# Kernel tuning notes

Measured on AMD Instinct MI355X. Metric: run time of the kernel, lower is better.

## Reference

```python
import jax, jax.numpy as jnp
import numpy as np

B, T, H, W, C = 2, 8, 64, 64, 128
NH, KT, KH, KW = 4, 3, 7, 7
HD = C // NH
SCALE = HD ** -0.5


def _starts(L, ks):
    i = jnp.arange(L)
    return jnp.clip(i - ks // 2, 0, L - ks)  # NATTEN border-clamped window start


def _na3d(q, k, v, rpb):
    # q,k,v: [B,T,H,W,NH,HD]; rpb: [NH,2KT-1,2KH-1,2KW-1]
    st, sh, sw = _starts(T, KT), _starts(H, KH), _starts(W, KW)
    ot, oh, ow = jnp.meshgrid(jnp.arange(KT), jnp.arange(KH), jnp.arange(KW), indexing='ij')
    ot, oh, ow = ot.ravel(), oh.ravel(), ow.ravel()          # [K] kernel offsets, K=KT*KH*KW
    t_abs = st[None, :] + ot[:, None]                        # [K,T] absolute neighbor coords
    h_abs = sh[None, :] + oh[:, None]                        # [K,H]
    w_abs = sw[None, :] + ow[:, None]                        # [K,W]
    qs = q * SCALE
    it, ih, iw = jnp.arange(T), jnp.arange(H), jnp.arange(W)

    def score_step(_, idx):
        ta, ha, wa = idx
        kg = k[:, ta][:, :, ha][:, :, :, wa]                 # [B,T,H,W,NH,HD] shifted keys
        s = jnp.einsum('bthwnd,bthwnd->bthwn', qs, kg)
        rt = ta - it + (KT - 1)
        rh = ha - ih + (KH - 1)
        rw = wa - iw + (KW - 1)
        bias = rpb[:, rt][:, :, rh][:, :, :, rw]             # [NH,T,H,W]
        return None, s + jnp.transpose(bias, (1, 2, 3, 0))[None]

    _, scores = jax.lax.scan(score_step, None, (t_abs, h_abs, w_abs))  # [K,B,T,H,W,NH]
    attn = jax.nn.softmax(scores, axis=0)

    def av_step(acc, xs):
        a, ta, ha, wa = xs
        vg = v[:, ta][:, :, ha][:, :, :, wa]                 # [B,T,H,W,NH,HD]
        return acc + a[..., None] * vg, None

    out, _ = jax.lax.scan(av_step, jnp.zeros_like(q), (attn, t_abs, h_abs, w_abs))
    return out


def setup_inputs() -> dict:
    key = jax.random.key(0)
    ks = jax.random.split(key, 6)
    x = jax.random.normal(ks[0], (B, T, H, W, C), jnp.float32)
    y = jax.random.normal(ks[1], (B, T, H, W, C), jnp.float32)
    qv_w = jax.random.normal(ks[2], (C, 2 * C), jnp.float32) * 0.02
    qv_b = jnp.zeros((2 * C,), jnp.float32)
    k_w = jax.random.normal(ks[3], (C, C), jnp.float32) * 0.02
    k_b = jnp.zeros((C,), jnp.float32)
    proj_w = jax.random.normal(ks[4], (C, C), jnp.float32) * 0.02
    proj_b = jnp.zeros((C,), jnp.float32)
    rpb = jax.random.normal(ks[5], (NH, 2 * KT - 1, 2 * KH - 1, 2 * KW - 1), jnp.float32) * 0.02
    return {'x': x, 'y': y, 'qv_w': qv_w, 'qv_b': qv_b, 'k_w': k_w, 'k_b': k_b,
            'proj_w': proj_w, 'proj_b': proj_b, 'rpb': rpb}


def reference(x, y, qv_w, qv_b, k_w, k_b, proj_w, proj_b, rpb):
    qv = (x @ qv_w + qv_b).reshape(B, T, H, W, 2, NH, HD)
    q, v = qv[..., 0, :, :], qv[..., 1, :, :]
    k = (y @ k_w + k_b).reshape(B, T, H, W, NH, HD)
    o = _na3d(q, k, v, rpb).reshape(B, T, H, W, C)
    return o @ proj_w + proj_b
```

## Files before the change

kernel.cpp:

```cpp
#include <hip/hip_runtime.h>
#include <hip/hip_bf16.h>
#include <hip/hip_fp16.h>
#include <cmath>

#define Bv   2
#define Tv   8
#define Hv   64
#define Wv   64
#define MPOS (Bv*Tv*Hv*Wv)
#define SCALEv 0.17677669529663687f

#define U_H   14
#define U_W   14
#define UPOS  588

#define KOFF   0
#define VTOFF  37888
#define POFF2  77312
#define RPBOFF 158720
#define SMEM_BYTES 162112

#define KPAD 136

typedef __attribute__((ext_vector_type(8))) short bf16x8;
typedef __attribute__((ext_vector_type(4))) float f32x4;

__device__ __forceinline__ unsigned short f2bf16(float x) {
  return __builtin_bit_cast(unsigned short, __float2bfloat16(x));
}
__device__ __forceinline__ float bf2f(unsigned short h) {
  return __uint_as_float((unsigned)h << 16);
}
__device__ __forceinline__ float h2f(unsigned short h) {
  return __half2float(__builtin_bit_cast(__half, h));
}
__device__ __forceinline__ unsigned short f2h(float x) {
  return __builtin_bit_cast(unsigned short, __float2half(x));
}
__device__ __forceinline__ unsigned pk2(float a, float b) {
  return (unsigned)f2bf16(a) | ((unsigned)f2bf16(b) << 16);
}
__device__ __forceinline__ void gload_lds16(const void* gsrc, void* ldst) {
  __builtin_amdgcn_global_load_lds(
      (const __attribute__((address_space(1))) unsigned int*)gsrc,
      (__attribute__((address_space(3))) unsigned int*)ldst, 16, 0, 0);
}

__global__ __launch_bounds__(256) void preconvert(
    const float* __restrict__ qv_w, const float* __restrict__ k_w,
    const float* __restrict__ proj_w,
    ushort* __restrict__ wqvT, ushort* __restrict__ wkT,
    ushort* __restrict__ wpT_hi, ushort* __restrict__ wpT_lo) {
  const int id = blockIdx.x * 256 + threadIdx.x;
  if (id < 32768) {
    const int n = id >> 7, kk = id & 127;
    wqvT[n * KPAD + kk] = f2bf16(qv_w[kk * 256 + n]);
  } else if (id < 49152) {
    const int j = id - 32768;
    const int n = j >> 7, kk = j & 127;
    wkT[n * KPAD + kk] = f2bf16(k_w[kk * 128 + n]);
  } else {
    const int j = id - 49152;
    const int n = j >> 7, kk = j & 127;
    const float v = proj_w[kk * 128 + n];
    const unsigned short hi = f2bf16(v);
    wpT_hi[n * KPAD + kk] = hi;
    wpT_lo[n * KPAD + kk] = f2bf16(v - bf2f(hi));
  }
}

__global__ __launch_bounds__(512) void gemm_qvk(
    const float* __restrict__ x, const float* __restrict__ y,
    const ushort* __restrict__ wqvT, const ushort* __restrict__ wkT,
    const float* __restrict__ qv_b, const float* __restrict__ k_b,
    ushort* __restrict__ qbuf, ushort* __restrict__ vbuf,
    ushort* __restrict__ kbuf) {
  __shared__ ushort Ws[128 * KPAD];
  const int tid  = threadIdx.x;
  const int bx   = blockIdx.x;
  const int seg  = bx >> 9;
  const int row0 = (bx & 511) * 128;

  const float*  A    = (seg == 2) ? y : x;
  const ushort* W    = (seg == 0) ? wqvT : (seg == 1) ? wqvT + 128 * KPAD : wkT;
  const float*  bias = (seg == 0) ? qv_b : (seg == 1) ? qv_b + 128 : k_b;
  ushort*       outp = (seg == 0) ? qbuf : (seg == 1) ? vbuf : kbuf;
  const float   scale = (seg == 0) ? SCALEv : 1.0f;

  {
    const uint4* wg = (const uint4*)W;
    for (int i = tid; i < 2176; i += 512)
      gload_lds16(wg + i, (uint4*)Ws + i);
  }

  const int wv = tid >> 6, lane = tid & 63, quad = lane >> 4, l16 = lane & 15;
  const int arow = row0 + wv * 16 + l16;

  bf16x8 af[4];
#pragma unroll
  for (int kk = 0; kk < 4; ++kk) {
    const float4* ap = (const float4*)(A + (size_t)arow * 128 + kk * 32 + quad * 8);
    const float4 a = ap[0], b2 = ap[1];
    af[kk] = __builtin_bit_cast(bf16x8,
        make_uint4(pk2(a.x, a.y), pk2(a.z, a.w), pk2(b2.x, b2.y), pk2(b2.z, b2.w)));
  }
  __syncthreads();

  f32x4 C[8];
#pragma unroll
  for (int nt = 0; nt < 8; ++nt) C[nt] = (f32x4){0.f, 0.f, 0.f, 0.f};

#pragma unroll
  for (int kk = 0; kk < 4; ++kk) {
#pragma unroll
    for (int nt = 0; nt < 8; ++nt) {
      const bf16x8 b2 = *(const bf16x8*)(Ws + (nt * 16 + l16) * KPAD + kk * 32 + quad * 8);
      C[nt] = __builtin_amdgcn_mfma_f32_16x16x32_bf16(af[kk], b2, C[nt], 0, 0, 0);
    }
  }

#pragma unroll
  for (int nt = 0; nt < 8; ++nt) {
    const int col = nt * 16 + l16;
    const float bv = bias[col];
#pragma unroll
    for (int r2 = 0; r2 < 4; ++r2) {
      const size_t row = row0 + wv * 16 + quad * 4 + r2;
      outp[row * 128 + col] = f2bf16((C[nt][r2] + bv) * scale);
    }
  }
}

__global__ __launch_bounds__(512) void gemm_proj_mfma(
    const float* __restrict__ o, const ushort* __restrict__ wpT_hi,
    const ushort* __restrict__ wpT_lo, const float* __restrict__ proj_b,
    float* __restrict__ out) {
  __shared__ ushort Wh[128 * KPAD];
  __shared__ ushort Wl[128 * KPAD];
  const int tid  = threadIdx.x;
  const int row0 = blockIdx.x * 128;
  {
    const uint4* wgh = (const uint4*)wpT_hi;
    const uint4* wgl = (const uint4*)wpT_lo;
    for (int i = tid; i < 2176; i += 512) {
      gload_lds16(wgh + i, (uint4*)Wh + i);
      gload_lds16(wgl + i, (uint4*)Wl + i);
    }
  }

  const int wv = tid >> 6, lane = tid & 63, quad = lane >> 4, l16 = lane & 15;
  const int arow = row0 + wv * 16 + l16;

  bf16x8 ah[4], al[4];
#pragma unroll
  for (int kk = 0; kk < 4; ++kk) {
    const float4* ap = (const float4*)(o + (size_t)arow * 128 + kk * 32 + quad * 8);
    const float4 a = ap[0], b2 = ap[1];
    const float vs[8] = {a.x, a.y, a.z, a.w, b2.x, b2.y, b2.z, b2.w};
    unsigned hw[4], lw[4];
#pragma unroll
    for (int e = 0; e < 4; ++e) {
      const unsigned short h0 = f2bf16(vs[2 * e]);
      const unsigned short h1 = f2bf16(vs[2 * e + 1]);
      hw[e] = (unsigned)h0 | ((unsigned)h1 << 16);
      lw[e] = (unsigned)f2bf16(vs[2 * e] - bf2f(h0)) |
              ((unsigned)f2bf16(vs[2 * e + 1] - bf2f(h1)) << 16);
    }
    ah[kk] = __builtin_bit_cast(bf16x8, make_uint4(hw[0], hw[1], hw[2], hw[3]));
    al[kk] = __builtin_bit_cast(bf16x8, make_uint4(lw[0], lw[1], lw[2], lw[3]));
  }
  __syncthreads();

  f32x4 C[8];
#pragma unroll
  for (int nt = 0; nt < 8; ++nt) C[nt] = (f32x4){0.f, 0.f, 0.f, 0.f};

#pragma unroll
  for (int kk = 0; kk < 4; ++kk) {
#pragma unroll
    for (int nt = 0; nt < 8; ++nt) {
      const int boff = (nt * 16 + l16) * KPAD + kk * 32 + quad * 8;
      const bf16x8 bh = *(const bf16x8*)(Wh + boff);
      const bf16x8 bl = *(const bf16x8*)(Wl + boff);
      C[nt] = __builtin_amdgcn_mfma_f32_16x16x32_bf16(ah[kk], bh, C[nt], 0, 0, 0);
      C[nt] = __builtin_amdgcn_mfma_f32_16x16x32_bf16(ah[kk], bl, C[nt], 0, 0, 0);
      C[nt] = __builtin_amdgcn_mfma_f32_16x16x32_bf16(al[kk], bh, C[nt], 0, 0, 0);
    }
  }

#pragma unroll
  for (int nt = 0; nt < 8; ++nt) {
    const int col = nt * 16 + l16;
    const float bv = proj_b[col];
#pragma unroll
    for (int r2 = 0; r2 < 4; ++r2) {
      const size_t row = row0 + wv * 16 + quad * 4 + r2;
      out[row * 128 + col] = C[nt][r2] + bv;
    }
  }
}

__global__ __launch_bounds__(1024, 1)
void na3d_tile(
    const ushort* __restrict__ qin,
    const ushort* __restrict__ kin,
    const ushort* __restrict__ vin,
    const float* __restrict__ rpb,
    float* __restrict__ oout) {
  __shared__ __align__(16) unsigned char smem[SMEM_BYTES];

  const int tid  = threadIdx.x;
  const int wv   = tid >> 6;
  const int lane = tid & 63;
  const int quad = lane >> 4;
  const int l16  = lane & 15;

  const int bx   = blockIdx.x;
  const int head = bx & 3;
  const int tile = bx >> 2;
  const int w0 = (tile & 7) << 3;
  const int h0 = ((tile >> 3) & 7) << 3;
  const int t  = (tile >> 6) & 7;
  const int b  = tile >> 9;

  const int st  = min(max(t - 1, 0), Tv - 3);
  const int u_h = min(max(h0 - 3, 0), Hv - U_H);
  const int u_w = min(max(w0 - 3, 0), Wv - U_W);
  const int rt_b = st - t + 2;

  const int mtile = wv & 3;
  bf16x8 afrag;
  {
    const int q_a  = mtile * 16 + l16;
    const int qh_a = h0 + (q_a >> 3), qw_a = w0 + (q_a & 7);
    const size_t qpos_a = ((size_t)(b * Tv + t) * Hv + qh_a) * Wv + qw_a;
    afrag = *(const bf16x8*)(qin + qpos_a * 128 + head * 32 + quad * 8);
  }

  float rv0 = 0.f;
  if (tid < 845) rv0 = rpb[head * 845 + tid];

  uint4 vv[3];
#pragma unroll
  for (int it = 0; it < 3; ++it) {
    const int j = tid + it * 1024;
    if (j < UPOS * 4) {
      const int pos = j >> 2, c = j & 3;
      const int ta = pos / 196;
      const int r  = pos - ta * 196;
      const int rh = r / 14;
      const int ha = u_h + rh;
      const int wa = u_w + (r - rh * 14);
      const size_t gpos = (((size_t)(b * Tv + st + ta) * Hv + ha) * Wv + wa);
      vv[it] = ((const uint4*)vin)[gpos * 16 + head * 4 + c];
    }
  }

  for (int ch = wv; ch < 37; ch += 16) {
    const int m = ch * 64 + lane;
    int pos = m >> 2;
    const int slot = m & 3;
    if (pos > UPOS - 1) pos = UPOS - 1;
    const int c  = (slot - (pos >> 2)) & 3;
    const int ta = pos / 196;
    const int r  = pos - ta * 196;
    const int rh = r / 14;
    const int ha = u_h + rh;
    const int wa = u_w + (r - rh * 14);
    const size_t gpos = (((size_t)(b * Tv + st + ta) * Hv + ha) * Wv + wa);
    gload_lds16((const uint4*)kin + gpos * 16 + head * 4 + c,
                smem + KOFF + ch * 1024 + lane * 16);
  }

#pragma unroll
  for (int it = 0; it < 3; ++it) {
    const int j = tid + it * 1024;
    if (j < UPOS * 4) {
      const int pos = j >> 2, c = j & 3;
      const unsigned sw = (unsigned)c << 5;
      const unsigned v4[4] = {vv[it].x, vv[it].y, vv[it].z, vv[it].w};
#pragma unroll
      for (int m2 = 0; m2 < 4; ++m2) {
        const int d0 = 8 * c + 2 * m2;
        const unsigned base = (unsigned)d0 * 1232 + (unsigned)pos * 2;
        *(ushort*)(smem + VTOFF + (base ^ sw))          = (ushort)(v4[m2] & 0xffffu);
        *(ushort*)(smem + VTOFF + ((base + 1232) ^ sw)) = (ushort)(v4[m2] >> 16);
      }
    }
  }
  if (tid < 448) {
    const int d = tid / 14, jj = tid - d * 14;
    const unsigned base = (unsigned)d * 1232 + 1176u + (unsigned)jj * 4;
    *(unsigned*)(smem + VTOFF + (base ^ (((unsigned)d >> 3) << 5))) = 0u;
  }
  if (tid < 845) ((float*)(smem + RPBOFF))[tid] = rv0;
  __syncthreads();

  {
    ushort* ph = (ushort*)(smem + POFF2);
    for (int nt = (wv >> 2); nt < 37; nt += 4) {
      const int u = nt * 16 + l16;
      const int slot = (quad + (u >> 2)) & 3;
      const bf16x8 bfrag = *(const bf16x8*)(smem + KOFF + u * 64 + slot * 16);
      f32x4 c = {0.f, 0.f, 0.f, 0.f};
      c = __builtin_amdgcn_mfma_f32_16x16x32_bf16(afrag, bfrag, c, 0, 0, 0);
#pragma unroll
      for (int r2 = 0; r2 < 4; ++r2) {
        const int qrow = mtile * 16 + quad * 4 + r2;
        ph[(size_t)qrow * 616 + u] = f2h(c[r2]);
      }
    }
  }
  __syncthreads();

  {
    const int qs = tid >> 4, l16s = tid & 15;
    const int qh_s = h0 + (qs >> 3), qw_s = w0 + (qs & 7);
    const int sh_s = min(max(qh_s - 3, 0), Hv - 7);
    const int sw_s = min(max(qw_s - 3, 0), Wv - 7);
    const int dh_s = sh_s - u_h, dw_s = sw_s - u_w;
    const int rh0 = sh_s - qh_s + 6, rw0 = sw_s - qw_s + 6;
    const float* rpb_l = (const float*)(smem + RPBOFF);
    ushort* Prow = (ushort*)(smem + POFF2 + (size_t)qs * 1232);

    const int utA = l16s / 7, aA = l16s - utA * 7;
    const int u0A = utA * 196 + (dh_s + aA) * 14 + dw_s;
    const float* bbA = rpb_l + (rt_b + utA) * 169 + (rh0 + aA) * 13 + rw0;
    const bool hasB = (l16s < 5);
    const int aB = l16s + 2;
    const int u0B = 2 * 196 + (dh_s + aB) * 14 + dw_s;
    const float* bbB = rpb_l + (rt_b + 2) * 169 + (rh0 + aB) * 13 + rw0;

    float exA[7], exB[7];
    float sum = 0.f;
#pragma unroll
    for (int e = 0; e < 7; ++e) {
      const float s = h2f(Prow[u0A + e]) + bbA[e];
      const float ex = __expf(s);
      exA[e] = ex; sum += ex;
    }
    if (hasB) {
#pragma unroll
      for (int e = 0; e < 7; ++e) {
        const float s = h2f(Prow[u0B + e]) + bbB[e];
        const float ex = __expf(s);
        exB[e] = ex; sum += ex;
      }
    }
    sum += __shfl_xor(sum, 1);
    sum += __shfl_xor(sum, 2);
    sum += __shfl_xor(sum, 4);
    sum += __shfl_xor(sum, 8);
    if (l16s == 0) ((float*)(smem + KOFF))[qs] = 1.0f / sum;
    __syncthreads();

    {
      uint4* Pv = (uint4*)Prow;
      for (int c = l16s; c < 77; c += 16) Pv[c] = make_uint4(0u, 0u, 0u, 0u);
    }
    __syncthreads();

#pragma unroll
    for (int e = 0; e < 7; ++e) Prow[u0A + e] = f2bf16(exA[e]);
    if (hasB) {
#pragma unroll
      for (int e = 0; e < 7; ++e) Prow[u0B + e] = f2bf16(exB[e]);
    }
  }
  __syncthreads();

  {
    const int khalf = wv >> 3;
    const int mtA = (wv >> 1) & 3;
    const int ntA = wv & 1;
    const int dcol = ntA * 16 + l16;
    const unsigned vlocal = (unsigned)dcol * 1232;
    const unsigned vsw = ((unsigned)(dcol >> 3) & 3u) << 5;
    const unsigned char* Abase = smem + POFF2 + (size_t)(mtA * 16 + l16) * 1232;
    f32x4 o = {0.f, 0.f, 0.f, 0.f};
    const int kt0 = khalf ? 10 : 0;
    const int kt1 = khalf ? 19 : 10;
#pragma unroll 4
    for (int kt = kt0; kt < kt1; ++kt) {
      const bf16x8 a  = *(const bf16x8*)(Abase + kt * 64 + quad * 16);
      const bf16x8 bb = *(const bf16x8*)(smem + VTOFF +
                          ((vlocal + kt * 64 + quad * 16) ^ vsw));
      o = __builtin_amdgcn_mfma_f32_16x16x32_bf16(a, bb, o, 0, 0, 0);
    }
    f32x4* part = (f32x4*)(smem + KOFF + 1024);
    if (khalf) part[(wv & 7) * 64 + lane] = o;
    __syncthreads();
    if (!khalf) {
      const f32x4 p2 = part[wv * 64 + lane];
      const float* invArr = (const float*)(smem + KOFF);
#pragma unroll
      for (int r2 = 0; r2 < 4; ++r2) {
        const int qrow = mtA * 16 + quad * 4 + r2;
        const float val = (o[r2] + p2[r2]) * invArr[qrow];
        const int qh2 = h0 + (qrow >> 3), qw2 = w0 + (qrow & 7);
        const size_t qp2 = ((size_t)(b * Tv + t) * Hv + qh2) * Wv + qw2;
        oout[qp2 * 128 + head * 32 + dcol] = val;
      }
    }
  }
}

extern "C" void kernel_launch(void* const* d_in, const int* in_sizes, int n_in,
                              void* d_out, int out_size, void* d_ws, size_t ws_size,
                              hipStream_t stream) {
  const float* x      = (const float*)d_in[0];
  const float* y      = (const float*)d_in[1];
  const float* qv_w   = (const float*)d_in[2];
  const float* qv_b   = (const float*)d_in[3];
  const float* k_w    = (const float*)d_in[4];
  const float* k_b    = (const float*)d_in[5];
  const float* proj_w = (const float*)d_in[6];
  const float* proj_b = (const float*)d_in[7];
  const float* rpb    = (const float*)d_in[8];
  float* out = (float*)d_out;

  const size_t elems = (size_t)MPOS * 128;
  ushort* qbuf = (ushort*)d_ws;
  ushort* kbuf = qbuf + elems;
  ushort* vbuf = kbuf + elems;
  float*  obuf = (float*)(vbuf + elems);
  ushort* wqvT   = (ushort*)(obuf + elems);
  ushort* wkT    = wqvT + 256 * KPAD;
  ushort* wpT_hi = wkT + 128 * KPAD;
  ushort* wpT_lo = wpT_hi + 128 * KPAD;

  preconvert    <<<256,  256, 0, stream>>>(qv_w, k_w, proj_w, wqvT, wkT, wpT_hi, wpT_lo);
  gemm_qvk      <<<1536, 512, 0, stream>>>(x, y, wqvT, wkT, qv_b, k_b, qbuf, vbuf, kbuf);
  na3d_tile     <<<4096, 1024, 0, stream>>>(qbuf, kbuf, vbuf, rpb, obuf);
  gemm_proj_mfma<<<512,  512, 0, stream>>>(obuf, wpT_hi, wpT_lo, proj_b, out);
}
```

Measured before the change: 284.4 us.

## Split neighborhood attention tile into two key passes to shrink LDS footprint

Restructures the na3d tile kernel to handle the 588-position key/value halo in two passes of about 320 positions. Each pass computes scores, partial softmax exponentials and a partial PV accumulation, and the row sum is finalized after the second pass. K fragments are now read straight from global memory instead of being staged in LDS. LDS drops from about 162 KB to about 75 KB so more than one 1024-thread block could fit per CU, at the cost of extra barriers, repeated index math and uncached global K loads.

```diff
diff --git a/kernel.cpp b/kernel.cpp
--- a/kernel.cpp
+++ b/kernel.cpp
@@ -14,11 +14,14 @@
 #define U_W   14
 #define UPOS  588
 
-#define KOFF   0
-#define VTOFF  37888
-#define POFF2  77312
-#define RPBOFF 158720
-#define SMEM_BYTES 162112
+#define SVT    656
+#define NCOL   328
+#define VTOFF  0
+#define POFF   20992
+#define RPBOFF 62976
+#define INVOFF 66368
+#define SCROFF 66624
+#define SMEM_BYTES 74816
 
 #define KPAD 136
 
@@ -200,7 +203,7 @@
   }
 }
 
-__global__ __launch_bounds__(1024, 1)
+__global__ __launch_bounds__(1024, 8)
 void na3d_tile(
     const ushort* __restrict__ qin,
     const ushort* __restrict__ kin,
@@ -236,163 +239,185 @@
     const size_t qpos_a = ((size_t)(b * Tv + t) * Hv + qh_a) * Wv + qw_a;
     afrag = *(const bf16x8*)(qin + qpos_a * 128 + head * 32 + quad * 8);
   }
-
-  float rv0 = 0.f;
-  if (tid < 845) rv0 = rpb[head * 845 + tid];
-
-  uint4 vv[3];
-#pragma unroll
-  for (int it = 0; it < 3; ++it) {
-    const int j = tid + it * 1024;
-    if (j < UPOS * 4) {
-      const int pos = j >> 2, c = j & 3;
-      const int ta = pos / 196;
-      const int r  = pos - ta * 196;
-      const int rh = r / 14;
-      const int ha = u_h + rh;
-      const int wa = u_w + (r - rh * 14);
-      const size_t gpos = (((size_t)(b * Tv + st + ta) * Hv + ha) * Wv + wa);
-      vv[it] = ((const uint4*)vin)[gpos * 16 + head * 4 + c];
-    }
-  }
-
-  for (int ch = wv; ch < 37; ch += 16) {
-    const int m = ch * 64 + lane;
-    int pos = m >> 2;
-    const int slot = m & 3;
-    if (pos > UPOS - 1) pos = UPOS - 1;
-    const int c  = (slot - (pos >> 2)) & 3;
-    const int ta = pos / 196;
-    const int r  = pos - ta * 196;
-    const int rh = r / 14;
-    const int ha = u_h + rh;
-    const int wa = u_w + (r - rh * 14);
-    const size_t gpos = (((size_t)(b * Tv + st + ta) * Hv + ha) * Wv + wa);
-    gload_lds16((const uint4*)kin + gpos * 16 + head * 4 + c,
-                smem + KOFF + ch * 1024 + lane * 16);
-  }
-
-#pragma unroll
-  for (int it = 0; it < 3; ++it) {
-    const int j = tid + it * 1024;
-    if (j < UPOS * 4) {
-      const int pos = j >> 2, c = j & 3;
-      const unsigned sw = (unsigned)c << 5;
-      const unsigned v4[4] = {vv[it].x, vv[it].y, vv[it].z, vv[it].w};
-#pragma unroll
-      for (int m2 = 0; m2 < 4; ++m2) {
-        const int d0 = 8 * c + 2 * m2;
-        const unsigned base = (unsigned)d0 * 1232 + (unsigned)pos * 2;
-        *(ushort*)(smem + VTOFF + (base ^ sw))          = (ushort)(v4[m2] & 0xffffu);
-        *(ushort*)(smem + VTOFF + ((base + 1232) ^ sw)) = (ushort)(v4[m2] >> 16);
-      }
-    }
-  }
-  if (tid < 448) {
-    const int d = tid / 14, jj = tid - d * 14;
-    const unsigned base = (unsigned)d * 1232 + 1176u + (unsigned)jj * 4;
-    *(unsigned*)(smem + VTOFF + (base ^ (((unsigned)d >> 3) << 5))) = 0u;
-  }
-  if (tid < 845) ((float*)(smem + RPBOFF))[tid] = rv0;
-  __syncthreads();
+  if (tid < 845) ((float*)(smem + RPBOFF))[tid] = rpb[head * 845 + tid];
+
+  const int qs = tid >> 4, l16s = tid & 15;
+  const int qh_s = h0 + (qs >> 3), qw_s = w0 + (qs & 7);
+  const int sh_s = min(max(qh_s - 3, 0), Hv - 7);
+  const int sw_s = min(max(qw_s - 3, 0), Wv - 7);
+  const int dh_s = sh_s - u_h, dw_s = sw_s - u_w;
+  const int rh0 = sh_s - qh_s + 6, rw0 = sw_s - qw_s + 6;
+  const int utA = l16s / 7, aA = l16s - utA * 7;
+  const int u0A = utA * 196 + (dh_s + aA) * 14 + dw_s;
+  const int bA  = (rt_b + utA) * 169 + (rh0 + aA) * 13 + rw0;
+  const bool hasB = (l16s < 5);
+  const int aB  = l16s + 2;
+  const int u0B = 392 + (dh_s + aB) * 14 + dw_s;
+  const int bB  = (rt_b + 2) * 169 + (rh0 + aB) * 13 + rw0;
+
+  const int khalf = wv >> 3, mtA = (wv >> 1) & 3, ntA = wv & 1;
+  const int dcol = ntA * 16 + l16;
+  const unsigned vsw = ((unsigned)(dcol >> 3) & 3u) << 5;
+
+  f32x4 o = {0.f, 0.f, 0.f, 0.f};
+  float sum = 0.f;
+
+#pragma unroll 1
+  for (int pass = 0; pass < 2; ++pass) {
+    const int lo   = pass ? 320 : 0;
+    const int nu   = pass ? 288 : 320;
+    const int NT   = pass ? 18  : 20;
+    const int nval = pass ? 268 : 320;
+
+    uint4 vv[2];
+    const int nchunk = nval * 4;
+#pragma unroll
+    for (int it = 0; it < 2; ++it) {
+      const int j = tid + it * 1024;
+      if (j < nchunk) {
+        const int pos = lo + (j >> 2), c = j & 3;
+        const int ta = pos / 196;
+        const int r  = pos - ta * 196;
+        const int rh = r / 14;
+        const int ha = u_h + rh;
+        const int wa = u_w + (r - rh * 14);
+        const size_t gpos = (((size_t)(b * Tv + st + ta) * Hv + ha) * Wv + wa);
+        vv[it] = ((const uint4*)vin)[gpos * 16 + head * 4 + c];
+      }
+    }
+
+    {
+      ushort* ph = (ushort*)(smem + POFF);
+      for (int nt = (wv >> 2); nt < NT; nt += 4) {
+        const int u = lo + nt * 16 + l16;
+        const int pos = min(u, UPOS - 1);
+        const int ta = pos / 196;
+        const int r  = pos - ta * 196;
+        const int rh = r / 14;
+        const int ha = u_h + rh;
+        const int wa = u_w + (r - rh * 14);
+        const size_t gpos = (((size_t)(b * Tv + st + ta) * Hv + ha) * Wv + wa);
+        const bf16x8 bfrag = *(const bf16x8*)(kin + gpos * 128 + head * 32 + quad * 8);
+        f32x4 c = {0.f, 0.f, 0.f, 0.f};
+        c = __builtin_amdgcn_mfma_f32_16x16x32_bf16(afrag, bfrag, c, 0, 0, 0);
+#pragma unroll
+        for (int r2 = 0; r2 < 4; ++r2) {
+          const int qrow = mtile * 16 + quad * 4 + r2;
+          ph[qrow * NCOL + (u - lo)] = f2h(c[r2]);
+        }
+      }
+    }
+
+#pragma unroll
+    for (int it = 0; it < 2; ++it) {
+      const int j = tid + it * 1024;
+      if (j < nchunk) {
+        const int pos2 = j >> 2, c = j & 3;
+        const unsigned sw = (unsigned)c << 5;
+        const unsigned v4[4] = {vv[it].x, vv[it].y, vv[it].z, vv[it].w};
+#pragma unroll
+        for (int m2 = 0; m2 < 4; ++m2) {
+          const int d0 = 8 * c + 2 * m2;
+          const unsigned base = (unsigned)d0 * SVT + (unsigned)pos2 * 2;
+          *(ushort*)(smem + VTOFF + (base ^ sw))         = (ushort)(v4[m2] & 0xffffu);
+          *(ushort*)(smem + VTOFF + ((base + SVT) ^ sw)) = (ushort)(v4[m2] >> 16);
+        }
+      }
+    }
+    if (pass == 1 && tid < 320) {
+      const int d = tid / 10, jj = tid - d * 10;
+      const unsigned base = (unsigned)d * SVT + 536u + (unsigned)jj * 4;
+      *(unsigned*)(smem + VTOFF + (base ^ (((unsigned)d >> 3) << 5))) = 0u;
+    }
+    __syncthreads();
+
+    unsigned pkA[4] = {0u, 0u, 0u, 0u}, pkB[4] = {0u, 0u, 0u, 0u};
+    {
+      const ushort* Ps = (const ushort*)(smem + POFF) + qs * NCOL;
+      const float* rpb_l = (const float*)(smem + RPBOFF);
+      const int hi = lo + nu;
+#pragma unroll
+      for (int e = 0; e < 7; ++e) {
+        const int u = u0A + e;
+        if (u >= lo && u < hi) {
+          const float s = h2f(Ps[u - lo]) + rpb_l[bA + e];
+          const float ex = __expf(s);
+          sum += ex;
+          pkA[e >> 1] |= (unsigned)f2bf16(ex) << ((e & 1) * 16);
+        }
+      }
+      if (hasB) {
+#pragma unroll
+        for (int e = 0; e < 7; ++e) {
+          const int u = u0B + e;
+          if (u >= lo && u < hi) {
+            const float s = h2f(Ps[u - lo]) + rpb_l[bB + e];
+            const float ex = __expf(s);
+            sum += ex;
+            pkB[e >> 1] |= (unsigned)f2bf16(ex) << ((e & 1) * 16);
+          }
+        }
+      }
+      if (pass == 1) {
+        float sm = sum;
+        sm += __shfl_xor(sm, 1);
+        sm += __shfl_xor(sm, 2);
+        sm += __shfl_xor(sm, 4);
+        sm += __shfl_xor(sm, 8);
+        if (l16s == 0) ((float*)(smem + INVOFF))[qs] = 1.0f / sm;
+      }
+    }
+    __syncthreads();
+
+    {
+      uint4* Pv = (uint4*)(smem + POFF + (size_t)qs * SVT);
+      for (int c = l16s; c < 41; c += 16) Pv[c] = make_uint4(0u, 0u, 0u, 0u);
+    }
+    __syncthreads();
+
+    {
+      ushort* Pr = (ushort*)(smem + POFF) + qs * NCOL;
+      const int hi = lo + nu;
+#pragma unroll
+      for (int e = 0; e < 7; ++e) {
+        const int u = u0A + e;
+        if (u >= lo && u < hi)
+          Pr[u - lo] = (ushort)(pkA[e >> 1] >> ((e & 1) * 16));
+      }
+      if (hasB) {
+#pragma unroll
+        for (int e = 0; e < 7; ++e) {
+          const int u = u0B + e;
+          if (u >= lo && u < hi)
+            Pr[u - lo] = (ushort)(pkB[e >> 1] >> ((e & 1) * 16));
+        }
+      }
+    }
+    __syncthreads();
+
+    {
+      const int ktn = pass ? 9 : 10;
+      const int kt0 = khalf * 5;
+      const int kt1 = khalf ? ktn : 5;
+      const unsigned char* Abase = smem + POFF + (size_t)(mtA * 16 + l16) * SVT;
+      const unsigned vlocal = (unsigned)dcol * SVT;
+      for (int kt = kt0; kt < kt1; ++kt) {
+        const bf16x8 a  = *(const bf16x8*)(Abase + kt * 64 + quad * 16);
+        const bf16x8 bb = *(const bf16x8*)(smem + VTOFF +
+                            ((vlocal + kt * 64 + quad * 16) ^ vsw));
+        o = __builtin_amdgcn_mfma_f32_16x16x32_bf16(a, bb, o, 0, 0, 0);
+      }
+    }
+    if (pass == 0) __syncthreads();
+  }
 
   {
-    ushort* ph = (ushort*)(smem + POFF2);
-    for (int nt = (wv >> 2); nt < 37; nt += 4) {
-      const int u = nt * 16 + l16;
-      const int slot = (quad + (u >> 2)) & 3;
-      const bf16x8 bfrag = *(const bf16x8*)(smem + KOFF + u * 64 + slot * 16);
-      f32x4 c = {0.f, 0.f, 0.f, 0.f};
-      c = __builtin_amdgcn_mfma_f32_16x16x32_bf16(afrag, bfrag, c, 0, 0, 0);
-#pragma unroll
-      for (int r2 = 0; r2 < 4; ++r2) {
-        const int qrow = mtile * 16 + quad * 4 + r2;
-        ph[(size_t)qrow * 616 + u] = f2h(c[r2]);
-      }
-    }
-  }
-  __syncthreads();
-
-  {
-    const int qs = tid >> 4, l16s = tid & 15;
-    const int qh_s = h0 + (qs >> 3), qw_s = w0 + (qs & 7);
-    const int sh_s = min(max(qh_s - 3, 0), Hv - 7);
-    const int sw_s = min(max(qw_s - 3, 0), Wv - 7);
-    const int dh_s = sh_s - u_h, dw_s = sw_s - u_w;
-    const int rh0 = sh_s - qh_s + 6, rw0 = sw_s - qw_s + 6;
-    const float* rpb_l = (const float*)(smem + RPBOFF);
-    ushort* Prow = (ushort*)(smem + POFF2 + (size_t)qs * 1232);
-
-    const int utA = l16s / 7, aA = l16s - utA * 7;
-    const int u0A = utA * 196 + (dh_s + aA) * 14 + dw_s;
-    const float* bbA = rpb_l + (rt_b + utA) * 169 + (rh0 + aA) * 13 + rw0;
-    const bool hasB = (l16s < 5);
-    const int aB = l16s + 2;
-    const int u0B = 2 * 196 + (dh_s + aB) * 14 + dw_s;
-    const float* bbB = rpb_l + (rt_b + 2) * 169 + (rh0 + aB) * 13 + rw0;
-
-    float exA[7], exB[7];
-    float sum = 0.f;
-#pragma unroll
-    for (int e = 0; e < 7; ++e) {
-      const float s = h2f(Prow[u0A + e]) + bbA[e];
-      const float ex = __expf(s);
-      exA[e] = ex; sum += ex;
-    }
-    if (hasB) {
-#pragma unroll
-      for (int e = 0; e < 7; ++e) {
-        const float s = h2f(Prow[u0B + e]) + bbB[e];
-        const float ex = __expf(s);
-        exB[e] = ex; sum += ex;
-      }
-    }
-    sum += __shfl_xor(sum, 1);
-    sum += __shfl_xor(sum, 2);
-    sum += __shfl_xor(sum, 4);
-    sum += __shfl_xor(sum, 8);
-    if (l16s == 0) ((float*)(smem + KOFF))[qs] = 1.0f / sum;
-    __syncthreads();
-
-    {
-      uint4* Pv = (uint4*)Prow;
-      for (int c = l16s; c < 77; c += 16) Pv[c] = make_uint4(0u, 0u, 0u, 0u);
-    }
-    __syncthreads();
-
-#pragma unroll
-    for (int e = 0; e < 7; ++e) Prow[u0A + e] = f2bf16(exA[e]);
-    if (hasB) {
-#pragma unroll
-      for (int e = 0; e < 7; ++e) Prow[u0B + e] = f2bf16(exB[e]);
-    }
-  }
-  __syncthreads();
-
-  {
-    const int khalf = wv >> 3;
-    const int mtA = (wv >> 1) & 3;
-    const int ntA = wv & 1;
-    const int dcol = ntA * 16 + l16;
-    const unsigned vlocal = (unsigned)dcol * 1232;
-    const unsigned vsw = ((unsigned)(dcol >> 3) & 3u) << 5;
-    const unsigned char* Abase = smem + POFF2 + (size_t)(mtA * 16 + l16) * 1232;
-    f32x4 o = {0.f, 0.f, 0.f, 0.f};
-    const int kt0 = khalf ? 10 : 0;
-    const int kt1 = khalf ? 19 : 10;
-#pragma unroll 4
-    for (int kt = kt0; kt < kt1; ++kt) {
-      const bf16x8 a  = *(const bf16x8*)(Abase + kt * 64 + quad * 16);
-      const bf16x8 bb = *(const bf16x8*)(smem + VTOFF +
-                          ((vlocal + kt * 64 + quad * 16) ^ vsw));
-      o = __builtin_amdgcn_mfma_f32_16x16x32_bf16(a, bb, o, 0, 0, 0);
-    }
-    f32x4* part = (f32x4*)(smem + KOFF + 1024);
+    f32x4* part = (f32x4*)(smem + SCROFF);
     if (khalf) part[(wv & 7) * 64 + lane] = o;
     __syncthreads();
     if (!khalf) {
       const f32x4 p2 = part[wv * 64 + lane];
-      const float* invArr = (const float*)(smem + KOFF);
+      const float* invArr = (const float*)(smem + INVOFF);
 #pragma unroll
       for (int r2 = 0; r2 < 4; ++r2) {
         const int qrow = mtA * 16 + quad * 4 + r2;
```

After: 443.1 us. 1.56x slower.
